# Kernel optimization log

Measured on AMD Instinct MI355X. Metric: run time of the kernel, lower is better.

## Reference

```python
import jax, jax.numpy as jnp
import numpy as np

B = 8          # batch
IMG = 224      # image side
W = 7          # window size
R = IMG // W   # window rows (32)
N = IMG * IMG  # tokens = 50176
D = 96         # model dim
H = 4          # heads
DH = 32        # dim per head
INNER = H * DH # 128
HID = 4 * D    # ffn hidden
EPS = 1e-5


def _rel_idx():
    pos = np.arange(W)
    gi, gj = np.meshgrid(pos, pos, indexing='ij')
    grid = np.stack([gi, gj], -1).reshape(-1, 2)          # (49, 2)
    rel = grid[:, None] - grid[None] + (W - 1)            # (49, 49, 2)
    return jnp.asarray(rel[..., 0] * (2 * W - 1) + rel[..., 1])  # (49, 49)

REL_IDX = _rel_idx()


def setup_inputs() -> dict:
    key = jax.random.key(0)
    ks = jax.random.split(key, 8)
    s = 0.02
    return {
        'x': jax.random.normal(ks[0], (B, N, D), jnp.float32),
        'w_qkv': jax.random.normal(ks[1], (3 * INNER, D), jnp.float32) * s,
        'w_out': jax.random.normal(ks[2], (D, INNER), jnp.float32) * s,
        'b_out': jnp.zeros((D,), jnp.float32),
        'rel_bias': jax.random.normal(ks[3], ((2 * W - 1) ** 2, H), jnp.float32) * s,
        'ln1_g': jnp.ones((D,), jnp.float32),
        'ln1_b': jnp.zeros((D,), jnp.float32),
        'ln2_g': jnp.ones((D,), jnp.float32),
        'ln2_b': jnp.zeros((D,), jnp.float32),
        'w1': jax.random.normal(ks[4], (HID, D), jnp.float32) * s,
        'b1': jnp.zeros((HID,), jnp.float32),
        'w2': jax.random.normal(ks[5], (D, HID), jnp.float32) * s,
        'b2': jnp.zeros((D,), jnp.float32),
    }


def _ln(x, g, b):
    m = jnp.mean(x, -1, keepdims=True)
    v = jnp.mean(jnp.square(x - m), -1, keepdims=True)
    return (x - m) * jax.lax.rsqrt(v + EPS) * g + b


def _forward(x, w_qkv, w_out, b_out, rel_bias, ln1_g, ln1_b, ln2_g, ln2_b, w1, b1, w2, b2):
    scale = DH ** -0.5
    # window partition: b (x w1 y w2) d -> (b x y) (w1 w2) d
    xw = x.reshape(B, R, W, R, W, D).transpose(0, 1, 3, 2, 4, 5).reshape(B * R * R, W * W, D)
    # PreNormResidual(Attention)
    h = _ln(xw, ln1_g, ln1_b)
    qkv = h @ w_qkv.T                                    # (bw, 49, 3*inner)
    q, k, v = jnp.split(qkv, 3, axis=-1)
    split_heads = lambda t: t.reshape(-1, W * W, H, DH).transpose(0, 2, 1, 3)
    q, k, v = split_heads(q), split_heads(k), split_heads(v)
    bias = rel_bias[REL_IDX].transpose(2, 0, 1)          # (H, 49, 49)
    dots = (jnp.einsum('bhid,bhjd->bhij', q, k) + bias[None]) * scale
    attn = jax.nn.softmax(dots, axis=-1)
    o = jnp.einsum('bhij,bhjd->bhid', attn, v)
    o = o.transpose(0, 2, 1, 3).reshape(-1, W * W, INNER)
    xw = o @ w_out.T + b_out + xw
    # expose: (b x y) (w1 w2) d -> b (x w1 y w2) d
    y = xw.reshape(B, R, R, W, W, D).transpose(0, 1, 3, 2, 4, 5).reshape(B, N, D)
    # PreNormResidual(FeedForward)
    h2 = _ln(y, ln2_g, ln2_b)
    h2 = jax.nn.gelu(h2 @ w1.T + b1, approximate=False)
    return h2 @ w2.T + b2 + y


def reference(x, w_qkv, w_out, b_out, rel_bias, ln1_g, ln1_b, ln2_g, ln2_b, w1, b1, w2, b2):
    return _forward(x, w_qkv, w_out, b_out, rel_bias, ln1_g, ln1_b, ln2_g, ln2_b, w1, b1, w2, b2)
```

## Files before the change

kernel.cpp:

```cpp
#include <hip/hip_runtime.h>
#include <math.h>

#define NB    8
#define IMG   224
#define NTOK  (IMG*IMG)
#define DIM   96
#define INR   128
#define HIDN  384
#define WT    49
#define SCALE 0.17677669529663687f
#define QKS   72
#define OSS   136
#define TSS   200

typedef __attribute__((ext_vector_type(8))) short bf16x8;
typedef __attribute__((ext_vector_type(4))) float f32x4;
typedef __attribute__((ext_vector_type(4))) unsigned int u32x4;

#define MFMA16(a,b,c) __builtin_amdgcn_mfma_f32_16x16x32_bf16((a),(b),(c),0,0,0)

__device__ __forceinline__ short f2bf(float f) {
    unsigned u = __builtin_bit_cast(unsigned, f);
    u += 0x7fffu + ((u >> 16) & 1u);
    return (short)(u >> 16);
}

__device__ __forceinline__ unsigned pktrunc(float lo, float hi) {
    return (__builtin_bit_cast(unsigned, hi) & 0xFFFF0000u) |
           (__builtin_bit_cast(unsigned, lo) >> 16);
}

__device__ __forceinline__ float gelu_f(float z) {
    const float t = z * z;
    const float u = z * fmaf(0.07135482f, t, 1.5957691f);
    return z / (1.f + __expf(-u));
}

__device__ __forceinline__ bf16x8 ldfrag(const short* base, int tile, int lane) {
    return *reinterpret_cast<const bf16x8*>(base + ((tile << 6) + lane) * 8);
}

__global__ void prep_kernel(const float* __restrict__ wqkv, const float* __restrict__ wout,
                            const float* __restrict__ w1,   const float* __restrict__ w2,
                            const float* __restrict__ rel_bias, char* __restrict__ ws)
{
    short* wqkvb = (short*)ws;
    short* woutb = (short*)(ws + 73728);
    short* w1b   = (short*)(ws + 98304);
    short* w2b   = (short*)(ws + 172032);
    float* biasp = (float*)(ws + 245760);
    const int idx = blockIdx.x * 256 + threadIdx.x;
    if (idx < 36864) {
        const int tile = idx >> 9, lane = (idx >> 3) & 63, j = idx & 7;
        const int r = tile / 3, c = tile % 3;
        wqkvb[idx] = f2bf(wqkv[(r*16 + (lane & 15))*96 + c*32 + (lane >> 4)*8 + j]);
    } else if (idx < 49152) {
        const int t = idx - 36864;
        const int tile = t >> 9, lane = (t >> 3) & 63, j = t & 7;
        const int r = tile >> 2, c = tile & 3;
        woutb[t] = f2bf(wout[(r*16 + (lane & 15))*128 + c*32 + (lane >> 4)*8 + j]);
    } else if (idx < 86016) {
        const int t = idx - 49152;
        const int tile = t >> 9, lane = (t >> 3) & 63, j = t & 7;
        const int r = tile / 3, c = tile % 3;
        w1b[t] = f2bf(w1[(r*16 + (lane & 15))*96 + c*32 + (lane >> 4)*8 + j]);
    } else if (idx < 122880) {
        const int t = idx - 86016;
        const int tile = t >> 9, lane = (t >> 3) & 63, j = t & 7;
        const int r = tile / 12, c = tile % 12;
        w2b[t] = f2bf(w2[(r*16 + (lane & 15))*384 + c*32 + (lane >> 4)*8 + j]);
    } else if (idx < 135424) {
        const int t = idx - 122880;
        const int h = t / 3136, r = t % 3136, q = r / 64, k = r % 64;
        float v = 0.f;
        if (k < 49) {
            const int rel = (q/7 - k/7 + 6) * 13 + (q%7 - k%7 + 6);
            v = rel_bias[rel * 4 + h] * SCALE;
        }
        biasp[t] = v;
    }
}

__global__ __launch_bounds__(256, 3) void fused_kernel(
    const float* __restrict__ x, const char* __restrict__ ws,
    const float* __restrict__ b_out, const float* __restrict__ ln1_g,
    const float* __restrict__ ln1_b, const float* __restrict__ ln2_g,
    const float* __restrict__ ln2_b, const float* __restrict__ b1,
    const float* __restrict__ b2, float* __restrict__ y)
{
    __shared__ __align__(16) char pool[50176];
    short* hs = (short*)pool;
    short* qk = (short*)(pool + 13312);
    short* os = (short*)(pool + 13312);
    short* h2 = (short*)pool;
    short* ts = (short*)(pool + 13312);

    const short* wqkvb = (const short*)ws;
    const short* woutb = (const short*)(ws + 73728);
    const short* w1b   = (const short*)(ws + 98304);
    const short* w2b   = (const short*)(ws + 172032);
    const float* biasp = (const float*)(ws + 245760);

    const int tid = threadIdx.x;
    const int wv  = tid >> 6;
    const int lane = tid & 63;
    const int l15 = tid & 15;
    const int l4  = (tid & 63) >> 4;
    const int wid = blockIdx.x;
    const int b = wid >> 10, xr = (wid >> 5) & 31, yr = wid & 31;
    const int qkbase = wv * 64 * QKS;

    if (tid < 196) {
        const int i = tid >> 2, g = tid & 3;
        const float* xp = x + ((size_t)b * NTOK + (size_t)(xr*7 + i/7) * IMG + (yr*7 + i%7)) * DIM + g*24;
        float v[24]; float s = 0.f, s2 = 0.f;
        #pragma unroll
        for (int c = 0; c < 6; ++c) {
            const float4 t4 = *reinterpret_cast<const float4*>(xp + c*4);
            v[c*4+0]=t4.x; v[c*4+1]=t4.y; v[c*4+2]=t4.z; v[c*4+3]=t4.w;
            s  += t4.x + t4.y + t4.z + t4.w;
            s2 += t4.x*t4.x + t4.y*t4.y + t4.z*t4.z + t4.w*t4.w;
        }
        s  += __shfl_xor(s, 1);  s  += __shfl_xor(s, 2);
        s2 += __shfl_xor(s2, 1); s2 += __shfl_xor(s2, 2);
        const float mu = s * (1.f/96.f);
        const float rs = rsqrtf(s2 * (1.f/96.f) - mu*mu + 1e-5f);
        #pragma unroll
        for (int c = 0; c < 12; ++c) {
            const int d = g*24 + c*2;
            const float a0 = (v[c*2+0] - mu) * rs * ln1_g[d]   + ln1_b[d];
            const float a1 = (v[c*2+1] - mu) * rs * ln1_g[d+1] + ln1_b[d+1];
            *reinterpret_cast<unsigned*>(&hs[i*104 + d]) = pktrunc(a0, a1);
        }
    }
    for (int idx = tid; idx < 780; idx += 256)
        *reinterpret_cast<unsigned*>(&hs[49*104 + idx*2]) = 0;
    __syncthreads();

    {
        f32x4 acc[4][4];
        #pragma unroll
        for (int nt = 0; nt < 4; ++nt)
            #pragma unroll
            for (int mt = 0; mt < 4; ++mt)
                acc[nt][mt] = (f32x4){0.f,0.f,0.f,0.f};
        #pragma unroll
        for (int k3 = 0; k3 < 3; ++k3) {
            bf16x8 a4[4];
            #pragma unroll
            for (int mt = 0; mt < 4; ++mt)
                a4[mt] = *reinterpret_cast<const bf16x8*>(&hs[(mt*16 + l15)*104 + k3*32 + l4*8]);
            #pragma unroll
            for (int nt = 0; nt < 4; ++nt) {
                const int r = (nt < 2) ? wv*2 + nt : 8 + wv*2 + (nt-2);
                const bf16x8 bfr = ldfrag(wqkvb, r*3 + k3, lane);
                #pragma unroll
                for (int mt = 0; mt < 4; ++mt)
                    acc[nt][mt] = MFMA16(a4[mt], bfr, acc[nt][mt]);
            }
        }
        #pragma unroll
        for (int nt = 0; nt < 4; ++nt) {
            const int col0 = nt*16;
            #pragma unroll
            for (int mt = 0; mt < 4; ++mt)
                #pragma unroll
                for (int rg = 0; rg < 4; ++rg)
                    qk[qkbase + (mt*16 + l4*4 + rg)*QKS + col0 + l15] = f2bf(acc[nt][mt][rg]);
        }
    }

    u32x4 vfrag[2][2];
    {
        f32x4 accv[2][4];
        #pragma unroll
        for (int nv = 0; nv < 2; ++nv)
            #pragma unroll
            for (int mt = 0; mt < 4; ++mt)
                accv[nv][mt] = (f32x4){0.f,0.f,0.f,0.f};
        #pragma unroll
        for (int k3 = 0; k3 < 3; ++k3) {
            bf16x8 a4[4];
            #pragma unroll
            for (int mt = 0; mt < 4; ++mt)
                a4[mt] = *reinterpret_cast<const bf16x8*>(&hs[(mt*16 + l15)*104 + k3*32 + l4*8]);
            #pragma unroll
            for (int nv = 0; nv < 2; ++nv) {
                const bf16x8 bfr = ldfrag(wqkvb, (16 + wv*2 + nv)*3 + k3, lane);
                #pragma unroll
                for (int mt = 0; mt < 4; ++mt)
                    accv[nv][mt] = MFMA16(a4[mt], bfr, accv[nv][mt]);
            }
        }
        #pragma unroll
        for (int md = 0; md < 2; ++md)
            #pragma unroll
            for (int kst = 0; kst < 2; ++kst)
                vfrag[md][kst] = (u32x4){
                    pktrunc(accv[md][2*kst  ][0], accv[md][2*kst  ][1]),
                    pktrunc(accv[md][2*kst  ][2], accv[md][2*kst  ][3]),
                    pktrunc(accv[md][2*kst+1][0], accv[md][2*kst+1][1]),
                    pktrunc(accv[md][2*kst+1][2], accv[md][2*kst+1][3])};
    }

    f32x4 st[4][4];
    {
        bf16x8 kf[4], qf[4];
        #pragma unroll
        for (int mt = 0; mt < 4; ++mt)
            kf[mt] = *reinterpret_cast<const bf16x8*>(&qk[qkbase + (mt*16 + l15)*QKS + 32 + l4*8]);
        #pragma unroll
        for (int nt = 0; nt < 4; ++nt)
            qf[nt] = *reinterpret_cast<const bf16x8*>(&qk[qkbase + (nt*16 + l15)*QKS + l4*8]);
        #pragma unroll
        for (int mt = 0; mt < 4; ++mt)
            #pragma unroll
            for (int nt = 0; nt < 4; ++nt)
                st[mt][nt] = MFMA16(kf[mt], qf[nt], ((f32x4){0.f,0.f,0.f,0.f}));
    }
    __syncthreads();

    unsigned pk[4][4][2];
    #pragma unroll
    for (int nq = 0; nq < 4; ++nq) {
        const int qc = (nq*16 + l15) < WT ? (nq*16 + l15) : 48;
        const float* bp = biasp + (wv*49 + qc)*64;
        float v[13];
        #pragma unroll
        for (int mk = 0; mk < 3; ++mk) {
            const float4 b4 = *reinterpret_cast<const float4*>(&bp[mk*16 + l4*4]);
            v[mk*4+0] = fmaf(st[mk][nq][0], SCALE, b4.x);
            v[mk*4+1] = fmaf(st[mk][nq][1], SCALE, b4.y);
            v[mk*4+2] = fmaf(st[mk][nq][2], SCALE, b4.z);
            v[mk*4+3] = fmaf(st[mk][nq][3], SCALE, b4.w);
        }
        v[12] = (l4 == 0) ? fmaf(st[3][nq][0], SCALE, bp[48]) : -1e30f;
        float mx = v[0];
        #pragma unroll
        for (int t = 1; t < 13; ++t) mx = fmaxf(mx, v[t]);
        mx = fmaxf(mx, __shfl_xor(mx, 16));
        mx = fmaxf(mx, __shfl_xor(mx, 32));
        float sum = 0.f;
        #pragma unroll
        for (int t = 0; t < 13; ++t) { v[t] = __expf(v[t] - mx); sum += v[t]; }
        sum += __shfl_xor(sum, 16);
        sum += __shfl_xor(sum, 32);
        const float inv = 1.f / sum;
        #pragma unroll
        for (int mk = 0; mk < 3; ++mk) {
            pk[nq][mk][0] = pktrunc(v[mk*4+0]*inv, v[mk*4+1]*inv);
            pk[nq][mk][1] = pktrunc(v[mk*4+2]*inv, v[mk*4+3]*inv);
        }
        pk[nq][3][0] = pktrunc(v[12]*inv, 0.f);
        pk[nq][3][1] = 0u;
    }

    {
        f32x4 oc[2][4];
        #pragma unroll
        for (int md = 0; md < 2; ++md)
            #pragma unroll
            for (int nq = 0; nq < 4; ++nq)
                oc[md][nq] = (f32x4){0.f,0.f,0.f,0.f};
        #pragma unroll
        for (int kst = 0; kst < 2; ++kst) {
            #pragma unroll
            for (int nq = 0; nq < 4; ++nq) {
                const bf16x8 bp8 = __builtin_bit_cast(bf16x8,
                    (u32x4){pk[nq][2*kst][0], pk[nq][2*kst][1], pk[nq][2*kst+1][0], pk[nq][2*kst+1][1]});
                #pragma unroll
                for (int md = 0; md < 2; ++md)
                    oc[md][nq] = MFMA16(__builtin_bit_cast(bf16x8, vfrag[md][kst]), bp8, oc[md][nq]);
            }
        }
        #pragma unroll
        for (int md = 0; md < 2; ++md)
            #pragma unroll
            for (int nq = 0; nq < 4; ++nq) {
                const unsigned lo = pktrunc(oc[md][nq][0], oc[md][nq][1]);
                const unsigned hi = pktrunc(oc[md][nq][2], oc[md][nq][3]);
                *reinterpret_cast<unsigned long long*>(
                    &os[(nq*16 + l15)*OSS + wv*32 + md*16 + l4*4]) =
                    ((unsigned long long)hi << 32) | lo;
            }
    }

    float xres[6][4];
    #pragma unroll
    for (int nt = 0; nt < 6; ++nt)
        #pragma unroll
        for (int rg = 0; rg < 4; ++rg) {
            const int tok = wv*16 + l4*4 + rg;
            const int tokc = tok < WT ? tok : 48;
            xres[nt][rg] = x[((size_t)b * NTOK + (size_t)(xr*7 + tokc/7) * IMG + (yr*7 + tokc%7)) * DIM + nt*16 + l15];
        }
    bf16x8 wofr[4][3];
    float bo6[6], g6[6], be6[6], b26[6], b1p[6];
    #pragma unroll
    for (int nt = 0; nt < 6; ++nt) {
        bo6[nt] = b_out[nt*16 + l15];
        g6[nt]  = ln2_g[nt*16 + l15];
        be6[nt] = ln2_b[nt*16 + l15];
        b26[nt] = b2[nt*16 + l15];
    }
    #pragma unroll
    for (int nt = 0; nt < 3; ++nt)
        #pragma unroll
        for (int kst = 0; kst < 4; ++kst)
            wofr[kst][nt] = ldfrag(woutb, nt*4 + kst, lane);
    #pragma unroll
    for (int al = 0; al < 2; ++al)
        #pragma unroll
        for (int n3 = 0; n3 < 3; ++n3)
            b1p[al*3 + n3] = b1[al*192 + wv*48 + n3*16 + l15];
    __syncthreads();

    float yreg[6][4];
    {
        bf16x8 afr[4];
        #pragma unroll
        for (int kst = 0; kst < 4; ++kst)
            afr[kst] = *reinterpret_cast<const bf16x8*>(&os[(wv*16 + l15)*OSS + kst*32 + l4*8]);
        #pragma unroll
        for (int nt = 0; nt < 6; ++nt) {
            f32x4 acc = (f32x4){0.f,0.f,0.f,0.f};
            #pragma unroll
            for (int kst = 0; kst < 4; ++kst) {
                const bf16x8 wfr = (nt < 3) ? wofr[kst][nt] : ldfrag(woutb, nt*4 + kst, lane);
                acc = MFMA16(afr[kst], wfr, acc);
            }
            #pragma unroll
            for (int rg = 0; rg < 4; ++rg)
                yreg[nt][rg] = acc[rg] + bo6[nt] + xres[nt][rg];
        }
    }

    float mu4[4], rs4[4];
    #pragma unroll
    for (int rg = 0; rg < 4; ++rg) {
        float s = 0.f, s2 = 0.f;
        #pragma unroll
        for (int nt = 0; nt < 6; ++nt) { const float v = yreg[nt][rg]; s += v; s2 += v*v; }
        s  += __shfl_xor(s, 1);  s  += __shfl_xor(s, 2);  s  += __shfl_xor(s, 4);  s  += __shfl_xor(s, 8);
        s2 += __shfl_xor(s2, 1); s2 += __shfl_xor(s2, 2); s2 += __shfl_xor(s2, 4); s2 += __shfl_xor(s2, 8);
        const float m = s * (1.f/96.f);
        mu4[rg] = m;
        rs4[rg] = rsqrtf(s2 * (1.f/96.f) - m*m + 1e-5f);
    }
    #pragma unroll
    for (int nt = 0; nt < 6; ++nt)
        #pragma unroll
        for (int rg = 0; rg < 4; ++rg)
            h2[(wv*16 + l4*4 + rg)*104 + nt*16 + l15] =
                f2bf((yreg[nt][rg] - mu4[rg]) * rs4[rg] * g6[nt] + be6[nt]);
    __syncthreads();

    f32x4 acc2[6];
    #pragma unroll
    for (int nt = 0; nt < 6; ++nt) acc2[nt] = (f32x4){0.f,0.f,0.f,0.f};

    #pragma unroll
    for (int al = 0; al < 2; ++al) {
        bf16x8 af[3][4];
        #pragma unroll
        for (int k3 = 0; k3 < 3; ++k3)
            #pragma unroll
            for (int mt = 0; mt < 4; ++mt)
                af[k3][mt] = *reinterpret_cast<const bf16x8*>(&h2[(mt*16 + l15)*104 + k3*32 + l4*8]);
        #pragma unroll
        for (int n3 = 0; n3 < 3; ++n3) {
            const int r1 = al*12 + wv*3 + n3;
            f32x4 a1[4];
            #pragma unroll
            for (int mt = 0; mt < 4; ++mt) a1[mt] = (f32x4){0.f,0.f,0.f,0.f};
            #pragma unroll
            for (int k3 = 0; k3 < 3; ++k3) {
                const bf16x8 bf = ldfrag(w1b, r1*3 + k3, lane);
                #pragma unroll
                for (int mt = 0; mt < 4; ++mt)
                    a1[mt] = MFMA16(af[k3][mt], bf, a1[mt]);
            }
            const float bb = b1p[al*3 + n3];
            #pragma unroll
            for (int mt = 0; mt < 4; ++mt)
                #pragma unroll
                for (int rg = 0; rg < 4; ++rg)
                    ts[(mt*16 + l4*4 + rg)*TSS + wv*48 + n3*16 + l15] = f2bf(gelu_f(a1[mt][rg] + bb));
        }
        __syncthreads();
        bf16x8 at[6];
        #pragma unroll
        for (int kl = 0; kl < 6; ++kl)
            at[kl] = *reinterpret_cast<const bf16x8*>(&ts[(wv*16 + l15)*TSS + kl*32 + l4*8]);
        #pragma unroll
        for (int nt = 0; nt < 6; ++nt) {
            #pragma unroll
            for (int kl = 0; kl < 6; ++kl)
                acc2[nt] = MFMA16(at[kl], ldfrag(w2b, nt*12 + al*6 + kl, lane), acc2[nt]);
        }
        if (al == 0) __syncthreads();
    }

    #pragma unroll
    for (int nt = 0; nt < 6; ++nt)
        #pragma unroll
        for (int rg = 0; rg < 4; ++rg) {
            const int tok = wv*16 + l4*4 + rg;
            if (tok < WT) {
                const size_t gi = ((size_t)b * NTOK + (size_t)(xr*7 + tok/7) * IMG + (yr*7 + tok%7)) * DIM + nt*16 + l15;
                y[gi] = acc2[nt][rg] + b26[nt] + yreg[nt][rg];
            }
        }
}

extern "C" void kernel_launch(void* const* d_in, const int* in_sizes, int n_in,
                              void* d_out, int out_size, void* d_ws, size_t ws_size,
                              hipStream_t stream) {
    const float* x     = (const float*)d_in[0];
    const float* w_qkv = (const float*)d_in[1];
    const float* w_out = (const float*)d_in[2];
    const float* b_out = (const float*)d_in[3];
    const float* rel_b = (const float*)d_in[4];
    const float* ln1_g = (const float*)d_in[5];
    const float* ln1_b = (const float*)d_in[6];
    const float* ln2_g = (const float*)d_in[7];
    const float* ln2_b = (const float*)d_in[8];
    const float* w1    = (const float*)d_in[9];
    const float* b1    = (const float*)d_in[10];
    const float* w2    = (const float*)d_in[11];
    const float* b2    = (const float*)d_in[12];
    float* y = (float*)d_out;
    char* ws = (char*)d_ws;

    prep_kernel<<<529, 256, 0, stream>>>(w_qkv, w_out, w1, w2, rel_b, ws);
    fused_kernel<<<NB * 32 * 32, 256, 0, stream>>>(x, ws, b_out, ln1_g, ln1_b,
                                                   ln2_g, ln2_b, b1, b2, y);
}
```

Before: 422.0 us.

## Partition FFN first GEMM by token rows per wave to drop barriers

Changes the FFN hidden-layer GEMM so that each wave computes all 192 hidden columns for its own 16 token rows, instead of computing 48 columns for all 64 rows. Every wave then writes and reads only its own rows of the shared GELU buffer, which allows the two __syncthreads per chunk to be removed. The cost is that each wave now loads all W1 fragments (four times more weight-fragment loads per wave) and issues fewer independent MFMA chains, which gives less instruction-level parallelism.

```diff
diff --git a/kernel.cpp b/kernel.cpp
--- a/kernel.cpp
+++ b/kernel.cpp
@@ -295,7 +295,7 @@
             xres[nt][rg] = x[((size_t)b * NTOK + (size_t)(xr*7 + tokc/7) * IMG + (yr*7 + tokc%7)) * DIM + nt*16 + l15];
         }
     bf16x8 wofr[4][3];
-    float bo6[6], g6[6], be6[6], b26[6], b1p[6];
+    float bo6[6], g6[6], be6[6], b26[6];
     #pragma unroll
     for (int nt = 0; nt < 6; ++nt) {
         bo6[nt] = b_out[nt*16 + l15];
@@ -308,11 +308,6 @@
         #pragma unroll
         for (int kst = 0; kst < 4; ++kst)
             wofr[kst][nt] = ldfrag(woutb, nt*4 + kst, lane);
-    #pragma unroll
-    for (int al = 0; al < 2; ++al)
-        #pragma unroll
-        for (int n3 = 0; n3 < 3; ++n3)
-            b1p[al*3 + n3] = b1[al*192 + wv*48 + n3*16 + l15];
     __syncthreads();
 
     float yreg[6][4];
@@ -361,33 +356,21 @@
 
     #pragma unroll
     for (int al = 0; al < 2; ++al) {
-        bf16x8 af[3][4];
+        bf16x8 af[3];
         #pragma unroll
         for (int k3 = 0; k3 < 3; ++k3)
-            #pragma unroll
-            for (int mt = 0; mt < 4; ++mt)
-                af[k3][mt] = *reinterpret_cast<const bf16x8*>(&h2[(mt*16 + l15)*104 + k3*32 + l4*8]);
-        #pragma unroll
-        for (int n3 = 0; n3 < 3; ++n3) {
-            const int r1 = al*12 + wv*3 + n3;
-            f32x4 a1[4];
-            #pragma unroll
-            for (int mt = 0; mt < 4; ++mt) a1[mt] = (f32x4){0.f,0.f,0.f,0.f};
-            #pragma unroll
-            for (int k3 = 0; k3 < 3; ++k3) {
-                const bf16x8 bf = ldfrag(w1b, r1*3 + k3, lane);
-                #pragma unroll
-                for (int mt = 0; mt < 4; ++mt)
-                    a1[mt] = MFMA16(af[k3][mt], bf, a1[mt]);
-            }
-            const float bb = b1p[al*3 + n3];
-            #pragma unroll
-            for (int mt = 0; mt < 4; ++mt)
-                #pragma unroll
-                for (int rg = 0; rg < 4; ++rg)
-                    ts[(mt*16 + l4*4 + rg)*TSS + wv*48 + n3*16 + l15] = f2bf(gelu_f(a1[mt][rg] + bb));
-        }
-        __syncthreads();
+            af[k3] = *reinterpret_cast<const bf16x8*>(&h2[(wv*16 + l15)*104 + k3*32 + l4*8]);
+        #pragma unroll
+        for (int n12 = 0; n12 < 12; ++n12) {
+            f32x4 a1 = (f32x4){0.f,0.f,0.f,0.f};
+            #pragma unroll
+            for (int k3 = 0; k3 < 3; ++k3)
+                a1 = MFMA16(af[k3], ldfrag(w1b, (al*12 + n12)*3 + k3, lane), a1);
+            const float bb = b1[al*192 + n12*16 + l15];
+            #pragma unroll
+            for (int rg = 0; rg < 4; ++rg)
+                ts[(wv*16 + l4*4 + rg)*TSS + n12*16 + l15] = f2bf(gelu_f(a1[rg] + bb));
+        }
         bf16x8 at[6];
         #pragma unroll
         for (int kl = 0; kl < 6; ++kl)
@@ -398,7 +381,6 @@
             for (int kl = 0; kl < 6; ++kl)
                 acc2[nt] = MFMA16(at[kl], ldfrag(w2b, nt*12 + al*6 + kl, lane), acc2[nt]);
         }
-        if (al == 0) __syncthreads();
     }
 
     #pragma unroll
```

Result: faster. 352.0 us (-16.6%).
